# Optimization experiments

Hardware: AMD Instinct MI355X
Metric: run time of the kernel (lower is better)

Reference implementation:

```python
import jax, jax.numpy as jnp
import numpy as np

B, C, H, W = 4, 256, 160, 160
N = 512
REID = 128
NUM_LAYERS = 2
BINS = 7          # adaptive_avg_pool2d target (7,7)
EPS_BN = 1e-5
EPS_NORM = 1e-12  # torch F.normalize eps


def setup_inputs() -> dict:
    key = jax.random.key(0)
    ks = jax.random.split(key, 8)
    x = jax.random.normal(ks[0], (B, C, H, W), jnp.float32)
    # valid normalized boxes: x1,y1 in [0,0.7], w,h in [0.1,0.3]
    xy1 = jax.random.uniform(ks[1], (B, N, 2), minval=0.0, maxval=0.7)
    wh = jax.random.uniform(ks[2], (B, N, 2), minval=0.1, maxval=0.3)
    bboxes = jnp.concatenate([xy1, jnp.minimum(xy1 + wh, 1.0)], axis=-1)
    # conv stack params (kaiming-ish init), BN in eval mode with running stats
    conv_w = jax.random.normal(ks[3], (NUM_LAYERS, C, C, 3, 3), jnp.float32) * np.sqrt(2.0 / (C * 9)).astype(np.float32)
    conv_b = jnp.zeros((NUM_LAYERS, C), jnp.float32)
    bn_gamma = jnp.ones((NUM_LAYERS, C), jnp.float32)
    bn_beta = jnp.zeros((NUM_LAYERS, C), jnp.float32)
    bn_mean = jnp.zeros((NUM_LAYERS, C), jnp.float32)
    bn_var = jnp.ones((NUM_LAYERS, C), jnp.float32)
    # reid_embedding MLP: Linear(C, C//2) -> ReLU -> Dropout(eval) -> Linear(C//2, REID)
    w1 = jax.random.normal(ks[4], (C // 2, C), jnp.float32) * 0.01
    b1 = jnp.zeros((C // 2,), jnp.float32)
    w2 = jax.random.normal(ks[5], (REID, C // 2), jnp.float32) * 0.01
    b2 = jnp.zeros((REID,), jnp.float32)
    return dict(x=x, bboxes=bboxes, conv_w=conv_w, conv_b=conv_b,
                bn_gamma=bn_gamma, bn_beta=bn_beta, bn_mean=bn_mean, bn_var=bn_var,
                w1=w1, b1=b1, w2=w2, b2=b2)


def _conv_bn_relu(x, w, b, gamma, beta, mean, var):
    y = jax.lax.conv_general_dilated(
        x, w, window_strides=(1, 1), padding=((1, 1), (1, 1)),
        dimension_numbers=('NCHW', 'OIHW', 'NCHW')) + b[None, :, None, None]
    scale = (gamma / jnp.sqrt(var + EPS_BN))[None, :, None, None]
    y = (y - mean[None, :, None, None]) * scale + beta[None, :, None, None]
    return jax.nn.relu(y)


def _roi_pool(S, box):
    # S: (C, H+1, W+1) integral image of the feature map; box: (4,) = x1,y1,x2,y2 in [0,1]
    x1 = jnp.clip(jnp.floor(box[0] * W).astype(jnp.int32), 0, W)
    y1 = jnp.clip(jnp.floor(box[1] * H).astype(jnp.int32), 0, H)
    x2 = jnp.clip(jnp.floor(box[2] * W).astype(jnp.int32), 0, W)
    y2 = jnp.clip(jnp.floor(box[3] * H).astype(jnp.int32), 0, H)
    valid = (x2 > x1) & (y2 > y1)
    hl = jnp.maximum(y2 - y1, 1)
    wl = jnp.maximum(x2 - x1, 1)
    i = jnp.arange(BINS)
    # PyTorch adaptive_avg_pool2d binning: [floor(i*L/B), ceil((i+1)*L/B))
    hs = y1 + (i * hl) // BINS
    he = y1 + ((i + 1) * hl + BINS - 1) // BINS
    ws = x1 + (i * wl) // BINS
    we = x1 + ((i + 1) * wl + BINS - 1) // BINS
    # bin sums via integral image -> (C, 7, 7)
    s = (S[:, he[:, None], we[None, :]] - S[:, hs[:, None], we[None, :]]
         - S[:, he[:, None], ws[None, :]] + S[:, hs[:, None], ws[None, :]])
    area = ((he - hs)[:, None] * (we - ws)[None, :]).astype(S.dtype)
    # adaptive 7x7 avg pool, then global avg pool over the 7x7 grid
    pooled = jnp.mean(s / area, axis=(1, 2))  # (C,)
    return pooled, valid


def reference(x, bboxes, conv_w, conv_b, bn_gamma, bn_beta, bn_mean, bn_var, w1, b1, w2, b2):
    f = x
    for l in range(NUM_LAYERS):
        f = _conv_bn_relu(f, conv_w[l], conv_b[l], bn_gamma[l], bn_beta[l], bn_mean[l], bn_var[l])
    # integral image, zero-padded: S[b,c,y,x] = sum of f[b,c,:y,:x] -> (B, C, H+1, W+1)
    S = jnp.pad(jnp.cumsum(jnp.cumsum(f, axis=2), axis=3), ((0, 0), (0, 0), (1, 0), (1, 0)))
    pooled, valid = jax.vmap(jax.vmap(_roi_pool, in_axes=(None, 0)), in_axes=(0, 0))(S, bboxes)
    # reid_embedding MLP (dropout is identity in eval)
    h = jax.nn.relu(jnp.einsum('bnc,hc->bnh', pooled, w1) + b1)
    feat = jnp.einsum('bnh,rh->bnr', h, w2) + b2
    feat = jnp.where(valid[..., None], feat, jnp.zeros((), feat.dtype))
    norm = jnp.maximum(jnp.linalg.norm(feat, axis=-1, keepdims=True), EPS_NORM)
    return feat / norm
```

## Files before the change

### kernel.cpp

```cpp
#include <hip/hip_runtime.h>
#include <hip/hip_bf16.h>

typedef __attribute__((ext_vector_type(8))) short s16x8;
typedef __attribute__((ext_vector_type(4))) float f32x4;


__device__ __forceinline__ void async_ld16(const void* g, void* l) {
  __builtin_amdgcn_global_load_lds(
      (const __attribute__((address_space(1))) void*)g,
      (__attribute__((address_space(3))) void*)l, 16, 0, 0);
}

__global__ __launch_bounds__(256) void prep_all(
    __hip_bfloat16* __restrict__ xpad, __hip_bfloat16* __restrict__ f1,
    const float* __restrict__ cw, __hip_bfloat16* __restrict__ wpk,
    const float* __restrict__ cb, const float* __restrict__ g,
    const float* __restrict__ bt, const float* __restrict__ mn,
    const float* __restrict__ vr, float* __restrict__ ab,
    const float* __restrict__ w1, const float* __restrict__ w2,
    float* __restrict__ w1t, float* __restrict__ w2t) {
  int bi = blockIdx.x;
  if (bi < 5152) {
    int buf = bi / 2576; int rem = bi - buf * 2576;
    int b = rem / 644;   int e = rem - b * 644;
    int y, x;
    if (e < 162)      { y = 0;           x = e; }
    else if (e < 324) { y = 161;         x = e - 162; }
    else if (e < 484) { y = e - 324 + 1; x = 0; }
    else              { y = e - 484 + 1; x = 161; }
    __hip_bfloat16* p = (buf ? f1 : xpad) + (((size_t)b * 162 + y) * 162 + x) * 256 + threadIdx.x;
    *p = __float2bfloat16(0.f);
  } else if (bi < 9760) {
    int t = (bi - 5152) * 256 + threadIdx.x;
    int ci = t & 255, co = (t >> 8) & 255, rest = t >> 16;
    int tap = rest % 9, l = rest / 9;
    int dy = tap / 3, dx = tap - dy * 3;
    float v = cw[((((size_t)l * 256 + co) * 256 + ci) * 3 + dy) * 3 + dx];
    wpk[(((size_t)l * 9 + tap) * 256 + co) * 256 + ci] = __float2bfloat16(v);
  } else if (bi < 9762) {
    int t = (bi - 9760) * 256 + threadIdx.x;
    float a = g[t] / sqrtf(vr[t] + 1e-5f);
    ab[t] = a;
    ab[512 + t] = (cb[t] - mn[t]) * a + bt[t];
  } else {
    int t = (bi - 9762) * 256 + threadIdx.x;
    if (t < 32768) {
      int h = t >> 8, k = t & 255;
      w1t[k * 128 + h] = w1[h * 256 + k];
    } else {
      int u = t - 32768;
      int r = u >> 7, k = u & 127;
      w2t[k * 128 + r] = w2[r * 128 + k];
    }
  }
}

__global__ __launch_bounds__(256) void nchw2nhwc(const float* __restrict__ x,
                                                 __hip_bfloat16* __restrict__ xpad) {
  __shared__ float tile[32][33];
  int blk = blockIdx.x;
  int xt = blk % 5;
  int ct = (blk / 5) & 7;
  int by = blk / 40;
  int b = by / 80, yp = by - (by / 80) * 80;
  int tx = threadIdx.x, ty = threadIdx.y;
#pragma unroll
  for (int ry = 0; ry < 2; ++ry) {
    int y = yp * 2 + ry;
    const float* src = x + (((size_t)(b * 256 + ct * 32)) * 160 + y) * 160 + xt * 32 + tx;
#pragma unroll
    for (int k = 0; k < 4; k++) tile[ty * 4 + k][tx] = src[(size_t)(ty * 4 + k) * 25600];
    __syncthreads();
    __hip_bfloat16* dst = xpad + (((size_t)(b * 162 + y + 1)) * 162 + (xt * 32 + 1)) * 256 + ct * 32 + tx;
#pragma unroll
    for (int k = 0; k < 4; k++) {
      int xx = ty * 4 + k;
      dst[(size_t)xx * 256] = __float2bfloat16(tile[tx][xx]);
    }
    __syncthreads();
  }
}

__global__ __launch_bounds__(256, 2) void conv_bn_relu(
    const __hip_bfloat16* __restrict__ inp, __hip_bfloat16* __restrict__ outp,
    const __hip_bfloat16* __restrict__ wpk,
    const float* __restrict__ alpha, const float* __restrict__ beff) {
  __shared__ __align__(16) short As[128 * 64];
  __shared__ __align__(16) short Bs[256 * 64];
  const int t = threadIdx.x;
  const int mtile = ((blockIdx.x & 7) * 100) + (blockIdx.x >> 3);
  const int l = t & 63;
  const int wv = t >> 6;
  const int lr = l & 15, lq = l >> 4;
  const int wm = wv >> 1, wn = wv & 1;

  const int srow = t >> 3;
  const int koff = (((t & 7) ^ (srow & 7)) << 3);
  const short* inS = (const short*)inp;
  const short* wS = (const short*)wpk;
  long abase[4];
#pragma unroll
  for (int i = 0; i < 4; i++) {
    int p = mtile * 128 + i * 32 + srow;
    int b = p / 25600; int r = p - b * 25600; int y = r / 160; int x = r - y * 160;
    abase[i] = (((long)b * 162 + y) * 162 + x) * 256 + koff;
  }
  const long bbase = ((long)srow) * 256 + koff;

  f32x4 acc[4][8];
#pragma unroll
  for (int i = 0; i < 4; i++)
#pragma unroll
    for (int j = 0; j < 8; j++) acc[i][j] = (f32x4){0.f, 0.f, 0.f, 0.f};

#pragma unroll 1
  for (int u = 0; u < 36; ++u) {
    const int tap = u >> 2, kc = u & 3;
    const int dy = tap / 3, dx = tap - dy * 3;
    const long aoff = ((long)(dy * 162 + dx)) * 256 + kc * 64;
    const long boff = (long)tap * 65536 + kc * 64;
    __syncthreads();
#pragma unroll
    for (int i = 0; i < 4; i++)
      async_ld16(inS + abase[i] + aoff, As + i * 2048 + t * 8);
#pragma unroll
    for (int j = 0; j < 8; j++)
      async_ld16(wS + bbase + boff + (long)j * 8192, Bs + j * 2048 + t * 8);
    __syncthreads();
#pragma unroll
    for (int kk = 0; kk < 2; ++kk) {
      const int ps = (((kk << 2) | lq) ^ (lr & 7)) << 3;
      s16x8 av[4], bv[8];
#pragma unroll
      for (int mi = 0; mi < 4; ++mi)
        av[mi] = *(const s16x8*)&As[(wm * 64 + mi * 16 + lr) * 64 + ps];
#pragma unroll
      for (int ni = 0; ni < 8; ++ni)
        bv[ni] = *(const s16x8*)&Bs[(wn * 128 + ni * 16 + lr) * 64 + ps];
#pragma unroll
      for (int mi = 0; mi < 4; ++mi)
#pragma unroll
        for (int ni = 0; ni < 8; ++ni)
          acc[mi][ni] = __builtin_amdgcn_mfma_f32_16x16x32_bf16(av[mi], bv[ni], acc[mi][ni], 0, 0, 0);
    }
  }

  float al[8], be_[8];
#pragma unroll
  for (int ni = 0; ni < 8; ++ni) {
    int co = wn * 128 + ni * 16 + lr;
    al[ni] = alpha[co];
    be_[ni] = beff[co];
  }
#pragma unroll
  for (int mi = 0; mi < 4; ++mi) {
    int prow = mtile * 128 + wm * 64 + mi * 16 + lq * 4;
#pragma unroll
    for (int j = 0; j < 4; ++j) {
      int p = prow + j;
      int b = p / 25600; int r = p - b * 25600; int y = r / 160; int x = r - y * 160;
      long ob = (((long)b * 162 + (y + 1)) * 162 + (x + 1)) * 256 + wn * 128;
#pragma unroll
      for (int ni = 0; ni < 8; ++ni) {
        float v = acc[mi][ni][j] * al[ni] + be_[ni];
        outp[ob + ni * 16 + lr] = __float2bfloat16(fmaxf(v, 0.f));
      }
    }
  }
}

__global__ __launch_bounds__(128) void cumsum_w(const __hip_bfloat16* __restrict__ f2,
                                                float* __restrict__ S) {
  int row = blockIdx.x;
  int b = row / 160, y = row - (row / 160) * 160;
  int cp = threadIdx.x;
  const unsigned* src =
      (const unsigned*)((const short*)f2 + (((size_t)b * 162 + y + 1) * 162 + 1) * 256) + cp;
  float2* dst = (float2*)(S + (((size_t)b * 161 + y + 1) * 161) * 256) + cp;
  dst[0] = float2{0.f, 0.f};
  float r0 = 0.f, r1 = 0.f;
  for (int x4 = 0; x4 < 160; x4 += 4) {
    unsigned v[4];
#pragma unroll
    for (int k = 0; k < 4; k++) v[k] = src[(size_t)(x4 + k) * 128];
#pragma unroll
    for (int k = 0; k < 4; k++) {
      r0 += __uint_as_float((v[k] & 0xffffu) << 16);
      r1 += __uint_as_float(v[k] & 0xffff0000u);
      dst[(size_t)(x4 + k + 1) * 128] = float2{r0, r1};
    }
  }
}

__global__ __launch_bounds__(256) void cumsum_h(float* __restrict__ S) {
  int bi = blockIdx.x;
  int b = bi / 161, q = bi - (bi / 161) * 161;
  int c = threadIdx.x;
  float* col = S + (((size_t)b * 161) * 161 + q) * 256 + c;
  const size_t ys = (size_t)161 * 256;
  col[0] = 0.f;
  float run = 0.f;
  for (int y0 = 1; y0 <= 160; y0 += 16) {
    float v[16];
#pragma unroll
    for (int k = 0; k < 16; k++) v[k] = col[(size_t)(y0 + k) * ys];
#pragma unroll
    for (int k = 0; k < 16; k++) { run += v[k]; col[(size_t)(y0 + k) * ys] = run; }
  }
}

__global__ __launch_bounds__(256) void roi_mlp(const float* __restrict__ S,
                                               const float* __restrict__ bbox,
                                               const float* __restrict__ w1t,
                                               const float* __restrict__ b1,
                                               const float* __restrict__ w2t,
                                               const float* __restrict__ b2,
                                               float* __restrict__ out) {
  int bn = blockIdx.x;
  int b = bn >> 9;
  int t = threadIdx.x;
  __shared__ float pl[256];
  __shared__ float hh[128];
  __shared__ float red[2];

  float bx1 = bbox[bn * 4 + 0], by1 = bbox[bn * 4 + 1];
  float bx2 = bbox[bn * 4 + 2], by2 = bbox[bn * 4 + 3];
  int x1 = min(max((int)floorf(bx1 * 160.f), 0), 160);
  int y1 = min(max((int)floorf(by1 * 160.f), 0), 160);
  int x2 = min(max((int)floorf(bx2 * 160.f), 0), 160);
  int y2 = min(max((int)floorf(by2 * 160.f), 0), 160);
  int vld = (x2 > x1 && y2 > y1) ? 1 : 0;
  int hl = max(y2 - y1, 1), wl = max(x2 - x1, 1);
  int hs[7], he[7], ws_[7], we_[7];
  float rh[7], rw[7];
#pragma unroll
  for (int i = 0; i < 7; i++) {
    hs[i] = y1 + (i * hl) / 7;
    he[i] = y1 + ((i + 1) * hl + 6) / 7;
    rh[i] = 1.f / (float)(he[i] - hs[i]);
    ws_[i] = x1 + (i * wl) / 7;
    we_[i] = x1 + ((i + 1) * wl + 6) / 7;
    rw[i] = 1.f / (float)(we_[i] - ws_[i]);
  }
  const float* Sb = S + (size_t)b * 161 * 161 * 256 + t;
  float acc = 0.f;
#pragma unroll
  for (int i = 0; i < 7; i++) {
    const float* rE = Sb + (size_t)he[i] * (161 * 256);
    const float* rS = Sb + (size_t)hs[i] * (161 * 256);
#pragma unroll
    for (int j = 0; j < 7; j++) {
      size_t qe = (size_t)we_[j] * 256, qs = (size_t)ws_[j] * 256;
      float s = rE[qe] - rS[qe] - rE[qs] + rS[qs];
      acc += s * (rh[i] * rw[j]);
    }
  }
  pl[t] = acc * (1.f / 49.f);
  __syncthreads();

  float a = 0.f;
  if (t < 128) {
    a = b1[t];
#pragma unroll 8
    for (int k = 0; k < 256; k++) a += w1t[k * 128 + t] * pl[k];
    hh[t] = fmaxf(a, 0.f);
  }
  __syncthreads();
  float f = 0.f;
  if (t < 128) {
    f = b2[t];
#pragma unroll 8
    for (int k = 0; k < 128; k++) f += w2t[k * 128 + t] * hh[k];
    if (!vld) f = 0.f;
    float ss = f * f;
#pragma unroll
    for (int off = 32; off > 0; off >>= 1) ss += __shfl_xor(ss, off);
    if ((t & 63) == 0) red[t >> 6] = ss;
  }
  __syncthreads();
  if (t < 128) {
    float nrm = fmaxf(sqrtf(red[0] + red[1]), 1e-12f);
    out[(size_t)bn * 128 + t] = f / nrm;
  }
}

extern "C" void kernel_launch(void* const* d_in, const int* in_sizes, int n_in,
                              void* d_out, int out_size, void* d_ws, size_t ws_size,
                              hipStream_t stream) {
  const float* x = (const float*)d_in[0];
  const float* bboxes = (const float*)d_in[1];
  const float* conv_w = (const float*)d_in[2];
  const float* conv_b = (const float*)d_in[3];
  const float* bn_g = (const float*)d_in[4];
  const float* bn_b = (const float*)d_in[5];
  const float* bn_m = (const float*)d_in[6];
  const float* bn_v = (const float*)d_in[7];
  const float* w1 = (const float*)d_in[8];
  const float* b1 = (const float*)d_in[9];
  const float* w2 = (const float*)d_in[10];
  const float* b2 = (const float*)d_in[11];

  char* ws = (char*)d_ws;
  const size_t PADB = (size_t)4 * 162 * 162 * 256 * 2;
  const size_t WPKB = (size_t)2 * 9 * 256 * 256 * 2;
  const size_t SB = (size_t)4 * 161 * 161 * 256 * 4;

  __hip_bfloat16* xpad = (__hip_bfloat16*)(ws);
  __hip_bfloat16* f1 = (__hip_bfloat16*)(ws + PADB);
  __hip_bfloat16* wpk = (__hip_bfloat16*)(ws + 2 * PADB);
  float* abuf = (float*)(ws + 2 * PADB + WPKB);
  float* S = (float*)(ws + 2 * PADB + WPKB + 4096);
  float* w1t = (float*)(ws + 2 * PADB + WPKB + 4096 + SB);
  float* w2t = w1t + 32768;

  prep_all<<<9954, 256, 0, stream>>>(xpad, f1, conv_w, wpk, conv_b, bn_g, bn_b, bn_m,
                                     bn_v, abuf, w1, w2, w1t, w2t);
  nchw2nhwc<<<12800, dim3(32, 8), 0, stream>>>(x, xpad);

  conv_bn_relu<<<800, 256, 0, stream>>>(xpad, f1, wpk, abuf, abuf + 512);
  conv_bn_relu<<<800, 256, 0, stream>>>(f1, xpad, wpk + (size_t)9 * 256 * 256, abuf + 256, abuf + 768);

  cumsum_w<<<640, 128, 0, stream>>>(xpad, S);
  cumsum_h<<<644, 256, 0, stream>>>(S);
  roi_mlp<<<2048, 256, 0, stream>>>(S, bboxes, w1t, b1, w2t, b2, (float*)d_out);
}
```

Baseline: 407.5 us.

## Switch conv GEMM to 32x32x16 MFMA and fuse layout transpose into prep kernel

The conv inner loop moves from 16x16x32 bf16 MFMA tiles (4x8 per wave) to 32x32x16 tiles (2x4 per wave). The larger tiles cut the number of LDS fragment loads and MFMA issues per K step. The epilogue is rewritten to match the 32x32 accumulator layout. Separately, the NCHW-to-NHWC transpose kernel is merged into the prep kernel to save one launch; the transpose blocks now share a launch with the padding and weight-packing work, which could change scheduling.

```diff
diff --git a/kernel.cpp b/kernel.cpp
--- a/kernel.cpp
+++ b/kernel.cpp
@@ -3,6 +3,7 @@
 
 typedef __attribute__((ext_vector_type(8))) short s16x8;
 typedef __attribute__((ext_vector_type(4))) float f32x4;
+typedef __attribute__((ext_vector_type(16))) float f32x16;
 
 
 __device__ __forceinline__ void async_ld16(const void* g, void* l) {
@@ -12,6 +13,7 @@
 }
 
 __global__ __launch_bounds__(256) void prep_all(
+    const float* __restrict__ x,
     __hip_bfloat16* __restrict__ xpad, __hip_bfloat16* __restrict__ f1,
     const float* __restrict__ cw, __hip_bfloat16* __restrict__ wpk,
     const float* __restrict__ cb, const float* __restrict__ g,
@@ -19,31 +21,56 @@
     const float* __restrict__ vr, float* __restrict__ ab,
     const float* __restrict__ w1, const float* __restrict__ w2,
     float* __restrict__ w1t, float* __restrict__ w2t) {
+  __shared__ float tile[32][33];
   int bi = blockIdx.x;
-  if (bi < 5152) {
-    int buf = bi / 2576; int rem = bi - buf * 2576;
+  if (bi < 12800) {
+    int blk = bi;
+    int xt = blk % 5;
+    int ct = (blk / 5) & 7;
+    int by = blk / 40;
+    int b = by / 80, yp = by - (by / 80) * 80;
+    int tx = threadIdx.x & 31, ty = threadIdx.x >> 5;
+#pragma unroll
+    for (int ry = 0; ry < 2; ++ry) {
+      int y = yp * 2 + ry;
+      const float* src = x + (((size_t)(b * 256 + ct * 32)) * 160 + y) * 160 + xt * 32 + tx;
+#pragma unroll
+      for (int k = 0; k < 4; k++) tile[ty * 4 + k][tx] = src[(size_t)(ty * 4 + k) * 25600];
+      __syncthreads();
+      __hip_bfloat16* dst =
+          xpad + (((size_t)(b * 162 + y + 1)) * 162 + (xt * 32 + 1)) * 256 + ct * 32 + tx;
+#pragma unroll
+      for (int k = 0; k < 4; k++) {
+        int xx = ty * 4 + k;
+        dst[(size_t)xx * 256] = __float2bfloat16(tile[tx][xx]);
+      }
+      __syncthreads();
+    }
+  } else if (bi < 17952) {
+    int e0 = bi - 12800;
+    int buf = e0 / 2576; int rem = e0 - buf * 2576;
     int b = rem / 644;   int e = rem - b * 644;
-    int y, x;
-    if (e < 162)      { y = 0;           x = e; }
-    else if (e < 324) { y = 161;         x = e - 162; }
-    else if (e < 484) { y = e - 324 + 1; x = 0; }
-    else              { y = e - 484 + 1; x = 161; }
-    __hip_bfloat16* p = (buf ? f1 : xpad) + (((size_t)b * 162 + y) * 162 + x) * 256 + threadIdx.x;
+    int y, xx;
+    if (e < 162)      { y = 0;           xx = e; }
+    else if (e < 324) { y = 161;         xx = e - 162; }
+    else if (e < 484) { y = e - 324 + 1; xx = 0; }
+    else              { y = e - 484 + 1; xx = 161; }
+    __hip_bfloat16* p = (buf ? f1 : xpad) + (((size_t)b * 162 + y) * 162 + xx) * 256 + threadIdx.x;
     *p = __float2bfloat16(0.f);
-  } else if (bi < 9760) {
-    int t = (bi - 5152) * 256 + threadIdx.x;
+  } else if (bi < 22560) {
+    int t = (bi - 17952) * 256 + threadIdx.x;
     int ci = t & 255, co = (t >> 8) & 255, rest = t >> 16;
-    int tap = rest % 9, l = rest / 9;
+    int tap = rest % 9, lyr = rest / 9;
     int dy = tap / 3, dx = tap - dy * 3;
-    float v = cw[((((size_t)l * 256 + co) * 256 + ci) * 3 + dy) * 3 + dx];
-    wpk[(((size_t)l * 9 + tap) * 256 + co) * 256 + ci] = __float2bfloat16(v);
-  } else if (bi < 9762) {
-    int t = (bi - 9760) * 256 + threadIdx.x;
+    float v = cw[((((size_t)lyr * 256 + co) * 256 + ci) * 3 + dy) * 3 + dx];
+    wpk[(((size_t)lyr * 9 + tap) * 256 + co) * 256 + ci] = __float2bfloat16(v);
+  } else if (bi < 22562) {
+    int t = (bi - 22560) * 256 + threadIdx.x;
     float a = g[t] / sqrtf(vr[t] + 1e-5f);
     ab[t] = a;
     ab[512 + t] = (cb[t] - mn[t]) * a + bt[t];
   } else {
-    int t = (bi - 9762) * 256 + threadIdx.x;
+    int t = (bi - 22562) * 256 + threadIdx.x;
     if (t < 32768) {
       int h = t >> 8, k = t & 255;
       w1t[k * 128 + h] = w1[h * 256 + k];
@@ -52,32 +79,6 @@
       int r = u >> 7, k = u & 127;
       w2t[k * 128 + r] = w2[r * 128 + k];
     }
-  }
-}
-
-__global__ __launch_bounds__(256) void nchw2nhwc(const float* __restrict__ x,
-                                                 __hip_bfloat16* __restrict__ xpad) {
-  __shared__ float tile[32][33];
-  int blk = blockIdx.x;
-  int xt = blk % 5;
-  int ct = (blk / 5) & 7;
-  int by = blk / 40;
-  int b = by / 80, yp = by - (by / 80) * 80;
-  int tx = threadIdx.x, ty = threadIdx.y;
-#pragma unroll
-  for (int ry = 0; ry < 2; ++ry) {
-    int y = yp * 2 + ry;
-    const float* src = x + (((size_t)(b * 256 + ct * 32)) * 160 + y) * 160 + xt * 32 + tx;
-#pragma unroll
-    for (int k = 0; k < 4; k++) tile[ty * 4 + k][tx] = src[(size_t)(ty * 4 + k) * 25600];
-    __syncthreads();
-    __hip_bfloat16* dst = xpad + (((size_t)(b * 162 + y + 1)) * 162 + (xt * 32 + 1)) * 256 + ct * 32 + tx;
-#pragma unroll
-    for (int k = 0; k < 4; k++) {
-      int xx = ty * 4 + k;
-      dst[(size_t)xx * 256] = __float2bfloat16(tile[tx][xx]);
-    }
-    __syncthreads();
   }
 }
 
@@ -91,7 +92,7 @@
   const int mtile = ((blockIdx.x & 7) * 100) + (blockIdx.x >> 3);
   const int l = t & 63;
   const int wv = t >> 6;
-  const int lr = l & 15, lq = l >> 4;
+  const int half = l >> 5, r5 = l & 31;
   const int wm = wv >> 1, wn = wv & 1;
 
   const int srow = t >> 3;
@@ -107,11 +108,13 @@
   }
   const long bbase = ((long)srow) * 256 + koff;
 
-  f32x4 acc[4][8];
-#pragma unroll
-  for (int i = 0; i < 4; i++)
-#pragma unroll
-    for (int j = 0; j < 8; j++) acc[i][j] = (f32x4){0.f, 0.f, 0.f, 0.f};
+  f32x16 acc[2][4];
+#pragma unroll
+  for (int i = 0; i < 2; i++)
+#pragma unroll
+    for (int j = 0; j < 4; j++)
+#pragma unroll
+      for (int e = 0; e < 16; e++) acc[i][j][e] = 0.f;
 
 #pragma unroll 1
   for (int u = 0; u < 36; ++u) {
@@ -128,42 +131,44 @@
       async_ld16(wS + bbase + boff + (long)j * 8192, Bs + j * 2048 + t * 8);
     __syncthreads();
 #pragma unroll
-    for (int kk = 0; kk < 2; ++kk) {
-      const int ps = (((kk << 2) | lq) ^ (lr & 7)) << 3;
-      s16x8 av[4], bv[8];
-#pragma unroll
-      for (int mi = 0; mi < 4; ++mi)
-        av[mi] = *(const s16x8*)&As[(wm * 64 + mi * 16 + lr) * 64 + ps];
-#pragma unroll
-      for (int ni = 0; ni < 8; ++ni)
-        bv[ni] = *(const s16x8*)&Bs[(wn * 128 + ni * 16 + lr) * 64 + ps];
-#pragma unroll
-      for (int mi = 0; mi < 4; ++mi)
-#pragma unroll
-        for (int ni = 0; ni < 8; ++ni)
-          acc[mi][ni] = __builtin_amdgcn_mfma_f32_16x16x32_bf16(av[mi], bv[ni], acc[mi][ni], 0, 0, 0);
-    }
-  }
-
-  float al[8], be_[8];
-#pragma unroll
-  for (int ni = 0; ni < 8; ++ni) {
-    int co = wn * 128 + ni * 16 + lr;
+    for (int kq = 0; kq < 4; ++kq) {
+      const int ps = (((kq << 1) | half) ^ (r5 & 7)) << 3;
+      s16x8 a2[2], b4[4];
+#pragma unroll
+      for (int mi = 0; mi < 2; ++mi)
+        a2[mi] = *(const s16x8*)&As[(wm * 64 + mi * 32 + r5) * 64 + ps];
+#pragma unroll
+      for (int ni = 0; ni < 4; ++ni)
+        b4[ni] = *(const s16x8*)&Bs[(wn * 128 + ni * 32 + r5) * 64 + ps];
+#pragma unroll
+      for (int mi = 0; mi < 2; ++mi)
+#pragma unroll
+        for (int ni = 0; ni < 4; ++ni)
+          acc[mi][ni] = __builtin_amdgcn_mfma_f32_32x32x16_bf16(a2[mi], b4[ni], acc[mi][ni], 0, 0, 0);
+    }
+  }
+
+  float al[4], be_[4];
+#pragma unroll
+  for (int ni = 0; ni < 4; ++ni) {
+    int co = wn * 128 + ni * 32 + r5;
     al[ni] = alpha[co];
     be_[ni] = beff[co];
   }
 #pragma unroll
-  for (int mi = 0; mi < 4; ++mi) {
-    int prow = mtile * 128 + wm * 64 + mi * 16 + lq * 4;
-#pragma unroll
-    for (int j = 0; j < 4; ++j) {
-      int p = prow + j;
-      int b = p / 25600; int r = p - b * 25600; int y = r / 160; int x = r - y * 160;
-      long ob = (((long)b * 162 + (y + 1)) * 162 + (x + 1)) * 256 + wn * 128;
-#pragma unroll
-      for (int ni = 0; ni < 8; ++ni) {
-        float v = acc[mi][ni][j] * al[ni] + be_[ni];
-        outp[ob + ni * 16 + lr] = __float2bfloat16(fmaxf(v, 0.f));
+  for (int mi = 0; mi < 2; ++mi) {
+#pragma unroll
+    for (int rg = 0; rg < 4; ++rg) {
+#pragma unroll
+      for (int rr = 0; rr < 4; ++rr) {
+        int p = mtile * 128 + wm * 64 + mi * 32 + 4 * half + 8 * rg + rr;
+        int b = p / 25600; int r = p - b * 25600; int y = r / 160; int x = r - y * 160;
+        long ob = (((long)b * 162 + (y + 1)) * 162 + (x + 1)) * 256 + wn * 128;
+#pragma unroll
+        for (int ni = 0; ni < 4; ++ni) {
+          float v = acc[mi][ni][rg * 4 + rr] * al[ni] + be_[ni];
+          outp[ob + ni * 32 + r5] = __float2bfloat16(fmaxf(v, 0.f));
+        }
       }
     }
   }
@@ -313,9 +318,8 @@
   float* w1t = (float*)(ws + 2 * PADB + WPKB + 4096 + SB);
   float* w2t = w1t + 32768;
 
-  prep_all<<<9954, 256, 0, stream>>>(xpad, f1, conv_w, wpk, conv_b, bn_g, bn_b, bn_m,
-                                     bn_v, abuf, w1, w2, w1t, w2t);
-  nchw2nhwc<<<12800, dim3(32, 8), 0, stream>>>(x, xpad);
+  prep_all<<<22754, 256, 0, stream>>>(x, xpad, f1, conv_w, wpk, conv_b, bn_g, bn_b, bn_m,
+                                      bn_v, abuf, w1, w2, w1t, w2t);
 
   conv_bn_relu<<<800, 256, 0, stream>>>(xpad, f1, wpk, abuf, abuf + 512);
   conv_bn_relu<<<800, 256, 0, stream>>>(f1, xpad, wpk + (size_t)9 * 256 * 256, abuf + 256, abuf + 768);
```

Result: slower. 443.3 us (+8.8%).
